# Optimization experiments

Measured on AMD Instinct MI355X. Metric: run time of the kernel, lower is better.

The kernel has to match this reference:

```python
import jax, jax.numpy as jnp
import numpy as np

H = 512   # hidden_dim
D = 512   # token feature dim (GRU input_size)
A = 256   # attn_dim
V = 10000 # vocab_size
TE = 256  # encoder timesteps
TD = 128  # decoder timesteps


def setup_inputs() -> dict:
    key = jax.random.key(0)
    ks = jax.random.split(key, 18)
    f = lambda k, shape, s: jax.random.normal(k, shape, jnp.float32) * s
    return {
        "x": f(ks[0], (1, TE, D), 1.0),
        "y": f(ks[1], (1, TD, D), 1.0),
        # encoder GRU params (PyTorch layout: gates [r|z|n] stacked)
        "Wi_e": f(ks[2], (3 * H, D), 0.04), "Wh_e": f(ks[3], (3 * H, H), 0.04),
        "bi_e": f(ks[4], (3 * H,), 0.04), "bh_e": f(ks[5], (3 * H,), 0.04),
        # decoder GRU params
        "Wi_d": f(ks[6], (3 * H, D), 0.04), "Wh_d": f(ks[7], (3 * H, H), 0.04),
        "bi_d": f(ks[8], (3 * H,), 0.04), "bh_d": f(ks[9], (3 * H,), 0.04),
        # additive attention params
        "Wh_attn": f(ks[10], (A, H), 0.06), "Ws_attn": f(ks[11], (A, H), 0.06),
        "b_attn": f(ks[12], (A,), 0.06), "v_attn": f(ks[13], (A,), 0.06),
        # output projections
        "W1": f(ks[14], (2 * V, 2 * H), 0.03), "b1": f(ks[15], (2 * V,), 0.03),
        "W2": f(ks[16], (V, 2 * V), 0.02), "b2": f(ks[17], (V,), 0.02),
    }


def _gru_gates(gi, gh, h):
    # gi/gh: [..., 3H] stacked input/hidden gate pre-activations, h: [..., H]
    ir, iz, inn = jnp.split(gi, 3, axis=-1)
    hr, hz, hn = jnp.split(gh, 3, axis=-1)
    r = jax.nn.sigmoid(ir + hr)
    z = jax.nn.sigmoid(iz + hz)
    n = jnp.tanh(inn + r * hn)
    return (1.0 - z) * n + z * h


def reference(x, y, Wi_e, Wh_e, bi_e, bh_e, Wi_d, Wh_d, bi_d, bh_d,
              Wh_attn, Ws_attn, b_attn, v_attn, W1, b1, W2, b2):
    X = x[0]  # [TE, D]
    Y = y[0]  # [TD, D]

    # Encoder: original calls self.encoder per single token with NO carried
    # hidden state, so each h_i is one GRU step from zero hidden. Vectorized:
    gi = X @ Wi_e.T + bi_e                      # [TE, 3H]
    gh = jnp.broadcast_to(bh_e, gi.shape)       # zero hidden -> only bias
    enc_H = _gru_gates(gi, gh, jnp.zeros((X.shape[0], H), X.dtype))  # [TE, H]
    h0 = enc_H[-1]                              # encoder_hidden_last

    # Decoder GRU over y with initial hidden h0
    def step(h, x_t):
        gi_t = x_t @ Wi_d.T + bi_d
        gh_t = h @ Wh_d.T + bh_d
        h_new = _gru_gates(gi_t, gh_t, h)
        return h_new, h_new

    _, dec_S = jax.lax.scan(step, h0, Y)        # [TD, H]

    # Bahdanau additive attention, fully batched over (TD, TE)
    encP = enc_H @ Wh_attn.T                    # [TE, A]
    decP = dec_S @ Ws_attn.T                    # [TD, A]
    e = jnp.tanh(encP[None, :, :] + decP[:, None, :] + b_attn)  # [TD, TE, A]
    scores = jnp.einsum('tea,a->te', e, v_attn)  # [TD, TE]
    attn = jax.nn.softmax(scores, axis=1)        # softmax over encoder steps
    context = attn @ enc_H                       # [TD, H]

    concat = jnp.concatenate([context, dec_S], axis=-1)  # [TD, 2H]
    out = concat @ W1.T + b1                     # [TD, 2V]
    out = out @ W2.T + b2                        # [TD, V]
    return out
```

## Files before the change

kernel.cpp:

```cpp
#include <hip/hip_runtime.h>
#include <stdint.h>

#define HID 512
#define THREE_H 1536
#define ADIM 256
#define NVOC 10000
#define TEnc 256
#define TDec 128

typedef float f32x4 __attribute__((ext_vector_type(4)));
typedef __bf16 bf16x8 __attribute__((ext_vector_type(8)));

__device__ __forceinline__ unsigned short f2bf(float f) {
  union { float f; unsigned u; } v; v.f = f;
  unsigned r = v.u + 0x7FFFu + ((v.u >> 16) & 1u);
  return (unsigned short)(r >> 16);
}
__device__ __forceinline__ float sigmoidf_(float x) { return 1.f / (1.f + __expf(-x)); }
__device__ __forceinline__ float tanh_fast(float x) {
  float ax = fabsf(x);
  float e = __expf(ax + ax);
  float t = 1.f - 2.f / (e + 1.f);
  return copysignf(t, x);
}

__device__ __forceinline__ void st_u64_sys(unsigned long long* p, unsigned long long v) {
  asm volatile("global_store_dwordx2 %0, %1, off sc0 sc1" :: "v"(p), "v"(v) : "memory");
}
__device__ __forceinline__ unsigned long long ld_u64_sys(const unsigned long long* p) {
  unsigned long long a;
  asm volatile("global_load_dwordx2 %0, %1, off sc0 sc1\n\ts_waitcnt vmcnt(0)"
               : "=&v"(a) : "v"(p) : "memory");
  return a;
}

#define GLDS16(gp, lp)                                                                 \
  __builtin_amdgcn_global_load_lds((const __attribute__((address_space(1))) void*)(gp),\
                                   (__attribute__((address_space(3))) void*)(lp), 16, 0, 0)

__global__ void cvt_xy(const float* __restrict__ x, const float* __restrict__ y,
                       unsigned short* __restrict__ xb, unsigned short* __restrict__ yb) {
  int i = (blockIdx.x * blockDim.x + threadIdx.x) * 4;
  const float* src;
  unsigned short* dst;
  int j;
  if (i < TEnc * HID) { src = x; dst = xb; j = i; }
  else { src = y; dst = yb; j = i - TEnc * HID; }
  float4 v = *(const float4*)(src + j);
  ushort4 o;
  o.x = f2bf(v.x); o.y = f2bf(v.y); o.z = f2bf(v.z); o.w = f2bf(v.w);
  *(ushort4*)(dst + j) = o;
}

template <int BN, int BK>
__global__ __launch_bounds__(256, 1) void gemm_bt(
    const unsigned short* __restrict__ Abf, const float* __restrict__ B,
    const float* __restrict__ bias, float* __restrict__ C, unsigned short* __restrict__ Cbf,
    int M, int N, int K) {
  constexpr int NF = BN / 16;
  constexpr int B4 = BN * BK / 1024;
  constexpr int AG = BK / 16;
  constexpr int KK = BK / 32;
  extern __shared__ char smem[];
  unsigned short* Al0 = (unsigned short*)smem;
  unsigned short* Al1 = Al0 + 128 * BK;
  unsigned short* Bl0 = Al1 + 128 * BK;
  unsigned short* Bl1 = Bl0 + BN * BK;

  const int tid = threadIdx.x;
  const int lane = tid & 63;
  const int wid = tid >> 6;
  const int m0 = blockIdx.x * 128;
  const int n0 = blockIdx.y * BN;
  const int NT = K / BK;

  float4 breg[B4];
  f32x4 acc[2][NF];
#pragma unroll
  for (int i = 0; i < 2; ++i)
#pragma unroll
    for (int j = 0; j < NF; ++j) acc[i][j] = (f32x4){0.f, 0.f, 0.f, 0.f};

  auto stageA = [&](int t, unsigned short* dst) {
    const unsigned short* Ab = Abf + (size_t)m0 * K + (size_t)t * BK;
#pragma unroll
    for (int g = 0; g < AG; ++g) {
      int elem = g * 2048 + tid * 8;
      int arow = elem / BK;
      int acol = elem - arow * BK;
      GLDS16(Ab + (size_t)arow * K + acol, (char*)dst + g * 4096 + wid * 1024);
    }
  };
  auto loadB = [&](int t) {
    const float* Bb = B + (size_t)t * BK;
#pragma unroll
    for (int p = 0; p < B4; ++p) {
      int e = (p * 256 + tid) * 4;
      int brow = e / BK;
      int bcol = e - brow * BK;
      int grow = n0 + brow;
      if (grow > N - 1) grow = N - 1;
      breg[p] = *(const float4*)(Bb + (size_t)grow * K + bcol);
    }
  };
  auto writeB = [&](unsigned short* dst) {
#pragma unroll
    for (int p = 0; p < B4; ++p) {
      ushort4 o;
      o.x = f2bf(breg[p].x); o.y = f2bf(breg[p].y);
      o.z = f2bf(breg[p].z); o.w = f2bf(breg[p].w);
      *(ushort4*)((char*)dst + (p * 256 + tid) * 8) = o;
    }
  };

  stageA(0, Al0);
  loadB(0);
  for (int t = 0; t < NT; ++t) {
    unsigned short* Ac = (t & 1) ? Al1 : Al0;
    unsigned short* Bc = (t & 1) ? Bl1 : Bl0;
    asm volatile("s_waitcnt vmcnt(0)" ::: "memory");
    writeB(Bc);
    __syncthreads();
    if (t + 1 < NT) {
      stageA(t + 1, (t & 1) ? Al0 : Al1);
      loadB(t + 1);
    }
    const int r0 = lane & 15;
    const int kb = (lane >> 4) * 8;
#pragma unroll
    for (int kk = 0; kk < KK; ++kk) {
      int ko = kk * 32 + kb;
      bf16x8 a0 = *(const bf16x8*)(Ac + (wid * 32 + r0) * BK + ko);
      bf16x8 a1 = *(const bf16x8*)(Ac + (wid * 32 + 16 + r0) * BK + ko);
#pragma unroll
      for (int nf = 0; nf < NF; ++nf) {
        bf16x8 bb = *(const bf16x8*)(Bc + (nf * 16 + r0) * BK + ko);
        acc[0][nf] = __builtin_amdgcn_mfma_f32_16x16x32_bf16(a0, bb, acc[0][nf], 0, 0, 0);
        acc[1][nf] = __builtin_amdgcn_mfma_f32_16x16x32_bf16(a1, bb, acc[1][nf], 0, 0, 0);
      }
    }
  }
  const int cc = lane & 15;
  const int rq = (lane >> 4) * 4;
#pragma unroll
  for (int mi = 0; mi < 2; ++mi) {
    int row = m0 + wid * 32 + mi * 16 + rq;
#pragma unroll
    for (int nf = 0; nf < NF; ++nf) {
      int col = n0 + nf * 16 + cc;
      if (col < N) {
        float bv = bias ? bias[col] : 0.f;
#pragma unroll
        for (int j = 0; j < 4; ++j) {
          float v = acc[mi][nf][j] + bv;
          if (C) C[(size_t)(row + j) * N + col] = v;
          if (Cbf) Cbf[(size_t)(row + j) * N + col] = f2bf(v);
        }
      }
    }
  }
}

__global__ __launch_bounds__(256, 1) void gemm_enc(
    const unsigned short* __restrict__ Abf, const float* __restrict__ Wi,
    const float* __restrict__ bi, const float* __restrict__ bh,
    float* __restrict__ encH, unsigned short* __restrict__ encHbf) {
  constexpr int BN = 96, BK = 128, NF = 6, B4 = 12, AG = 8, KK = 4, K = 512;
  extern __shared__ char smem[];
  unsigned short* Al0 = (unsigned short*)smem;
  unsigned short* Al1 = Al0 + 128 * BK;
  unsigned short* Bl0 = Al1 + 128 * BK;
  unsigned short* Bl1 = Bl0 + BN * BK;

  const int tid = threadIdx.x;
  const int lane = tid & 63;
  const int wid = tid >> 6;
  const int m0 = blockIdx.x * 128;
  const int n0g = blockIdx.y * 32;
  const int NT = K / BK;

  float4 breg[B4];
  f32x4 acc[2][NF];
#pragma unroll
  for (int i = 0; i < 2; ++i)
#pragma unroll
    for (int j = 0; j < NF; ++j) acc[i][j] = (f32x4){0.f, 0.f, 0.f, 0.f};

  auto stageA = [&](int t, unsigned short* dst) {
    const unsigned short* Ab = Abf + (size_t)m0 * K + (size_t)t * BK;
#pragma unroll
    for (int g = 0; g < AG; ++g) {
      int elem = g * 2048 + tid * 8;
      int arow = elem >> 7;
      int acol = elem & 127;
      GLDS16(Ab + (size_t)arow * K + acol, (char*)dst + g * 4096 + wid * 1024);
    }
  };
  auto loadB = [&](int t) {
    const float* Bb = Wi + (size_t)t * BK;
#pragma unroll
    for (int p = 0; p < B4; ++p) {
      int e = (p * 256 + tid) * 4;
      int brow = e >> 7;
      int bcol = e & 127;
      int grow = (brow >> 5) * HID + n0g + (brow & 31);
      breg[p] = *(const float4*)(Bb + (size_t)grow * K + bcol);
    }
  };
  auto writeB = [&](unsigned short* dst) {
#pragma unroll
    for (int p = 0; p < B4; ++p) {
      ushort4 o;
      o.x = f2bf(breg[p].x); o.y = f2bf(breg[p].y);
      o.z = f2bf(breg[p].z); o.w = f2bf(breg[p].w);
      *(ushort4*)((char*)dst + (p * 256 + tid) * 8) = o;
    }
  };

  stageA(0, Al0);
  loadB(0);
  for (int t = 0; t < NT; ++t) {
    unsigned short* Ac = (t & 1) ? Al1 : Al0;
    unsigned short* Bc = (t & 1) ? Bl1 : Bl0;
    asm volatile("s_waitcnt vmcnt(0)" ::: "memory");
    writeB(Bc);
    __syncthreads();
    if (t + 1 < NT) {
      stageA(t + 1, (t & 1) ? Al0 : Al1);
      loadB(t + 1);
    }
    const int r0 = lane & 15;
    const int kb = (lane >> 4) * 8;
#pragma unroll
    for (int kk = 0; kk < KK; ++kk) {
      int ko = kk * 32 + kb;
      bf16x8 a0 = *(const bf16x8*)(Ac + (wid * 32 + r0) * BK + ko);
      bf16x8 a1 = *(const bf16x8*)(Ac + (wid * 32 + 16 + r0) * BK + ko);
#pragma unroll
      for (int nf = 0; nf < NF; ++nf) {
        bf16x8 bb = *(const bf16x8*)(Bc + (nf * 16 + r0) * BK + ko);
        acc[0][nf] = __builtin_amdgcn_mfma_f32_16x16x32_bf16(a0, bb, acc[0][nf], 0, 0, 0);
        acc[1][nf] = __builtin_amdgcn_mfma_f32_16x16x32_bf16(a1, bb, acc[1][nf], 0, 0, 0);
      }
    }
  }
  const int cc = lane & 15;
  const int rq = (lane >> 4) * 4;
#pragma unroll
  for (int mi = 0; mi < 2; ++mi) {
    int row = m0 + wid * 32 + mi * 16 + rq;
#pragma unroll
    for (int nfj = 0; nfj < 2; ++nfj) {
      int j = n0g + nfj * 16 + cc;
      float br_ = bi[j] + bh[j];
      float bz_ = bi[HID + j] + bh[HID + j];
      float bin_ = bi[2 * HID + j];
      float bhn_ = bh[2 * HID + j];
#pragma unroll
      for (int jj = 0; jj < 4; ++jj) {
        float r = sigmoidf_(acc[mi][nfj][jj] + br_);
        float z = sigmoidf_(acc[mi][nfj + 2][jj] + bz_);
        float n = tanh_fast(acc[mi][nfj + 4][jj] + bin_ + r * bhn_);
        float h = (1.f - z) * n;
        encH[(size_t)(row + jj) * HID + j] = h;
        encHbf[(size_t)(row + jj) * HID + j] = f2bf(h);
      }
    }
  }
}

__global__ __launch_bounds__(256, 1) void gru_scan(
    const float* __restrict__ Whd, const float* __restrict__ bhd,
    const float* __restrict__ giY, const float* __restrict__ h0,
    unsigned long long* __restrict__ hx,
    unsigned short* __restrict__ decSbf, unsigned short* __restrict__ concatbf) {
  __shared__ float hl[548];
  __shared__ float dots[48];
  const int tid = threadIdx.x;
  const int lane = tid & 63, wid = tid >> 6;
  const int g = blockIdx.x;

  const int row16 = lane & 15;
  const int q = lane >> 4;
  float4 wreg[32];
  {
    int wrow = (wid < 3) ? wid : 0;
    const float* wr = Whd + ((size_t)wrow * HID + (size_t)g * 16 + row16) * HID + q * 128;
#pragma unroll
    for (int i = 0; i < 32; ++i) wreg[i] = *(const float4*)(wr + i * 4);
  }
  float bhr = 0.f, bhz = 0.f, bhn = 0.f, hreg = 0.f;
  if (wid == 3 && lane < 16) {
    int jj = g * 16 + lane;
    bhr = bhd[jj]; bhz = bhd[HID + jj]; bhn = bhd[2 * HID + jj];
    hreg = h0[jj];
  }
  {
    int w0 = tid * 2, w1 = tid * 2 + 1;
    hl[w0 + ((w0 >> 7) << 2)] = h0[w0];
    hl[w1 + ((w1 >> 7) << 2)] = h0[w1];
  }
  __syncthreads();

  for (int t = 0; t < TDec; ++t) {
    float gir = 0.f, giz = 0.f, gin = 0.f;
    if (wid < 3) {
      const float4* hp = (const float4*)hl;
      const int hb = q * 33;
      float p0 = 0.f, p1 = 0.f, p2 = 0.f, p3 = 0.f;
#pragma unroll
      for (int i = 0; i < 32; i += 4) {
        float4 ha = hp[hb + i], hv = hp[hb + i + 1], hc = hp[hb + i + 2], hd = hp[hb + i + 3];
        float4 wa = wreg[i], wb = wreg[i + 1], wc = wreg[i + 2], wd = wreg[i + 3];
        p0 += wa.x * ha.x + wa.y * ha.y + wa.z * ha.z + wa.w * ha.w;
        p1 += wb.x * hv.x + wb.y * hv.y + wb.z * hv.z + wb.w * hv.w;
        p2 += wc.x * hc.x + wc.y * hc.y + wc.z * hc.z + wc.w * hc.w;
        p3 += wd.x * hd.x + wd.y * hd.y + wd.z * hd.z + wd.w * hd.w;
      }
      float p = (p0 + p1) + (p2 + p3);
      p += __shfl_xor(p, 16);
      p += __shfl_xor(p, 32);
      if (lane < 16) dots[wid * 16 + lane] = p;
    } else if (lane < 16) {
      int jj = g * 16 + lane;
      const float* gi = giY + (size_t)t * THREE_H;
      gir = gi[jj]; giz = gi[HID + jj]; gin = gi[2 * HID + jj];
    }
    __syncthreads();
    unsigned long long* hxB = hx + (size_t)(t & 1) * 256;
    if (wid == 3 && lane < 16) {
      int jj = g * 16 + lane;
      float r = sigmoidf_(gir + dots[lane] + bhr);
      float z = sigmoidf_(giz + dots[16 + lane] + bhz);
      float n = tanh_fast(gin + r * (dots[32 + lane] + bhn));
      float hn = (1.f - z) * n + z * hreg;
      hreg = hn;
      unsigned short hb16 = f2bf(hn);
      unsigned short hb_up = (unsigned short)__shfl_xor((int)hb16, 1);
      if ((lane & 1) == 0) {
        unsigned long long w = ((unsigned long long)(unsigned)(t + 1) << 32) |
                               ((unsigned)hb_up << 16) | (unsigned)hb16;
        st_u64_sys(hxB + g * 8 + (lane >> 1), w);
      }
      decSbf[(size_t)t * HID + jj] = hb16;
      concatbf[(size_t)t * 2 * HID + HID + jj] = hb16;
    }
    if (t == TDec - 1) break;
    {
      const unsigned long long* p0 = hxB + tid;
      const unsigned tag = (unsigned)(t + 1);
      unsigned long long v;
      int guard = 0;
      do { v = ld_u64_sys(p0); } while ((unsigned)(v >> 32) != tag && ++guard < (1 << 20));
      int w0 = tid * 2, w1 = tid * 2 + 1;
      hl[w0 + ((w0 >> 7) << 2)] = __uint_as_float(((unsigned)v & 0xFFFFu) << 16);
      hl[w1 + ((w1 >> 7) << 2)] = __uint_as_float((((unsigned)v >> 16) & 0xFFFFu) << 16);
    }
    __syncthreads();
  }
}

__global__ __launch_bounds__(256) void attn_ctx(const float* __restrict__ encP,
                                                const float* __restrict__ decP,
                                                const float* __restrict__ vattn,
                                                const float* __restrict__ encH,
                                                unsigned short* __restrict__ concatbf) {
  __shared__ float dp[ADIM], vv[ADIM], pl[TEnc];
  __shared__ float red[8];
  const int t = blockIdx.x, tid = threadIdx.x;
  if (tid < 64) {
    *(float4*)(dp + tid * 4) = *(const float4*)(decP + (size_t)t * ADIM + tid * 4);
    *(float4*)(vv + tid * 4) = *(const float4*)(vattn + tid * 4);
  }
  __syncthreads();
  float s = 0.f;
  const float* ep = encP + (size_t)tid * ADIM;
#pragma unroll 4
  for (int a = 0; a < ADIM; a += 4) {
    float4 e4 = *(const float4*)(ep + a);
    s += vv[a] * tanh_fast(e4.x + dp[a]);
    s += vv[a + 1] * tanh_fast(e4.y + dp[a + 1]);
    s += vv[a + 2] * tanh_fast(e4.z + dp[a + 2]);
    s += vv[a + 3] * tanh_fast(e4.w + dp[a + 3]);
  }
  float m = s;
#pragma unroll
  for (int off = 32; off; off >>= 1) m = fmaxf(m, __shfl_xor(m, off));
  if ((tid & 63) == 0) red[tid >> 6] = m;
  __syncthreads();
  m = fmaxf(fmaxf(red[0], red[1]), fmaxf(red[2], red[3]));
  float p = __expf(s - m);
  pl[tid] = p;
  float sum = p;
#pragma unroll
  for (int off = 32; off; off >>= 1) sum += __shfl_xor(sum, off);
  if ((tid & 63) == 0) red[4 + (tid >> 6)] = sum;
  __syncthreads();
  float inv = 1.f / (red[4] + red[5] + red[6] + red[7]);
  float a0 = 0.f, a1 = 0.f;
  for (int e = 0; e < TEnc; ++e) {
    float pe = pl[e];
    a0 += pe * encH[(size_t)e * HID + tid];
    a1 += pe * encH[(size_t)e * HID + tid + 256];
  }
  concatbf[(size_t)t * 2 * HID + tid] = f2bf(a0 * inv);
  concatbf[(size_t)t * 2 * HID + tid + 256] = f2bf(a1 * inv);
}

extern "C" void kernel_launch(void* const* d_in, const int* in_sizes, int n_in,
                              void* d_out, int out_size, void* d_ws, size_t ws_size,
                              hipStream_t stream) {
  const float* x = (const float*)d_in[0];
  const float* y = (const float*)d_in[1];
  const float* Wi_e = (const float*)d_in[2];
  const float* bi_e = (const float*)d_in[4];
  const float* bh_e = (const float*)d_in[5];
  const float* Wi_d = (const float*)d_in[6];
  const float* Wh_d = (const float*)d_in[7];
  const float* bi_d = (const float*)d_in[8];
  const float* bh_d = (const float*)d_in[9];
  const float* Wh_attn = (const float*)d_in[10];
  const float* Ws_attn = (const float*)d_in[11];
  const float* b_attn = (const float*)d_in[12];
  const float* v_attn = (const float*)d_in[13];
  const float* W1 = (const float*)d_in[14];
  const float* b1 = (const float*)d_in[15];
  const float* W2 = (const float*)d_in[16];
  const float* b2 = (const float*)d_in[17];
  float* out = (float*)d_out;

  char* ws = (char*)d_ws;
  size_t off = 0;
  auto alloc = [&](size_t bytes) {
    char* p = ws + off;
    off += (bytes + 255) & ~(size_t)255;
    return p;
  };
  char* ctrl = alloc(4096);
  unsigned long long* hx = (unsigned long long*)ctrl;
  unsigned short* Xbf = (unsigned short*)alloc((size_t)TEnc * HID * 2);
  unsigned short* Ybf = (unsigned short*)alloc((size_t)TDec * HID * 2);
  float* giY = (float*)alloc((size_t)TDec * THREE_H * 4);
  float* encH = (float*)alloc((size_t)TEnc * HID * 4);
  unsigned short* encHbf = (unsigned short*)alloc((size_t)TEnc * HID * 2);
  float* encP = (float*)alloc((size_t)TEnc * ADIM * 4);
  float* decP = (float*)alloc((size_t)TDec * ADIM * 4);
  unsigned short* decSbf = (unsigned short*)alloc((size_t)TDec * HID * 2);
  unsigned short* concatbf = (unsigned short*)alloc((size_t)TDec * 2 * HID * 2);
  unsigned short* out1bf = (unsigned short*)alloc((size_t)TDec * 20000 * 2);

  hipMemsetAsync(ctrl, 0, 4096, stream);

  auto* g32 = gemm_bt<32, 128>;
  auto* g80 = gemm_bt<80, 128>;
  auto* g64 = gemm_bt<64, 160>;
  const int smem32 = (128 + 32) * 128 * 2 * 2;
  const int smem80 = (128 + 80) * 128 * 2 * 2;
  const int smem64 = (128 + 64) * 160 * 2 * 2;
  const int smemEnc = (128 + 96) * 128 * 2 * 2;
  hipFuncSetAttribute((const void*)g32, hipFuncAttributeMaxDynamicSharedMemorySize, smem32);
  hipFuncSetAttribute((const void*)g80, hipFuncAttributeMaxDynamicSharedMemorySize, smem80);
  hipFuncSetAttribute((const void*)g64, hipFuncAttributeMaxDynamicSharedMemorySize, smem64);
  hipFuncSetAttribute((const void*)gemm_enc, hipFuncAttributeMaxDynamicSharedMemorySize, smemEnc);

  cvt_xy<<<(TEnc + TDec) * HID / 1024, 256, 0, stream>>>(x, y, Xbf, Ybf);
  gemm_enc<<<dim3(2, 16), 256, smemEnc, stream>>>(Xbf, Wi_e, bi_e, bh_e, encH, encHbf);
  g32<<<dim3(2, 8), 256, smem32, stream>>>(encHbf, Wh_attn, nullptr, encP, nullptr, 256, 256, 512);
  g32<<<dim3(1, 48), 256, smem32, stream>>>(Ybf, Wi_d, bi_d, giY, nullptr, 128, 1536, 512);
  gru_scan<<<32, 256, 0, stream>>>(Wh_d, bh_d, giY, encH + 255 * HID, hx, decSbf, concatbf);
  g32<<<dim3(1, 8), 256, smem32, stream>>>(decSbf, Ws_attn, b_attn, decP, nullptr, 128, 256, 512);
  attn_ctx<<<TDec, 256, 0, stream>>>(encP, decP, v_attn, encH, concatbf);
  g80<<<dim3(1, 250), 256, smem80, stream>>>(concatbf, W1, b1, nullptr, out1bf, 128, 20000, 1024);
  g64<<<dim3(1, 157), 256, smem64, stream>>>(out1bf, W2, b2, out, nullptr, 128, NVOC, 20000);
}
```

Before: 601.1 us.

## Replicate GRU hidden-state mailbox per block and shrink W2 GEMM tile

The decoder GRU scan now writes each new hidden-state slice into 32 per-block copies of the exchange buffer. Each block polls its own private copy instead of all 32 blocks polling one shared buffer, which is meant to cut contention on the system-scope loads in the serial loop. The cost is 32 times more remote stores per step and a larger control buffer to clear. Separately, the final W2 GEMM tile width drops from 64 to 32 columns, doubling the grid to 313 blocks for better CU occupancy at the cost of less reuse of the A operand.

```diff
diff --git a/kernel.cpp b/kernel.cpp
--- a/kernel.cpp
+++ b/kernel.cpp
@@ -327,27 +327,35 @@
       gir = gi[jj]; giz = gi[HID + jj]; gin = gi[2 * HID + jj];
     }
     __syncthreads();
-    unsigned long long* hxB = hx + (size_t)(t & 1) * 256;
-    if (wid == 3 && lane < 16) {
-      int jj = g * 16 + lane;
-      float r = sigmoidf_(gir + dots[lane] + bhr);
-      float z = sigmoidf_(giz + dots[16 + lane] + bhz);
-      float n = tanh_fast(gin + r * (dots[32 + lane] + bhn));
-      float hn = (1.f - z) * n + z * hreg;
-      hreg = hn;
-      unsigned short hb16 = f2bf(hn);
-      unsigned short hb_up = (unsigned short)__shfl_xor((int)hb16, 1);
-      if ((lane & 1) == 0) {
-        unsigned long long w = ((unsigned long long)(unsigned)(t + 1) << 32) |
-                               ((unsigned)hb_up << 16) | (unsigned)hb16;
-        st_u64_sys(hxB + g * 8 + (lane >> 1), w);
-      }
-      decSbf[(size_t)t * HID + jj] = hb16;
-      concatbf[(size_t)t * 2 * HID + HID + jj] = hb16;
+    unsigned long long* hxB = hx + (size_t)(t & 1) * (32 * 256);
+    if (wid == 3) {
+      unsigned long long wval = 0;
+      if (lane < 16) {
+        int jj = g * 16 + lane;
+        float r = sigmoidf_(gir + dots[lane] + bhr);
+        float z = sigmoidf_(giz + dots[16 + lane] + bhz);
+        float n = tanh_fast(gin + r * (dots[32 + lane] + bhn));
+        float hn = (1.f - z) * n + z * hreg;
+        hreg = hn;
+        unsigned short hb16 = f2bf(hn);
+        unsigned short hb_up = (unsigned short)__shfl_xor((int)hb16, 1);
+        wval = ((unsigned long long)(unsigned)(t + 1) << 32) |
+               ((unsigned)hb_up << 16) | (unsigned)hb16;
+        decSbf[(size_t)t * HID + jj] = hb16;
+        concatbf[(size_t)t * 2 * HID + HID + jj] = hb16;
+      }
+      if (t < TDec - 1) {
+        unsigned long long bw = __shfl(wval, 2 * (lane & 7));
+        const int c0 = lane >> 3;
+        const int wofs = g * 8 + (lane & 7);
+#pragma unroll
+        for (int rep = 0; rep < 4; ++rep)
+          st_u64_sys(hxB + (size_t)(c0 + rep * 8) * 256 + wofs, bw);
+      }
     }
     if (t == TDec - 1) break;
     {
-      const unsigned long long* p0 = hxB + tid;
+      const unsigned long long* p0 = hxB + (size_t)g * 256 + tid;
       const unsigned tag = (unsigned)(t + 1);
       unsigned long long v;
       int guard = 0;
@@ -436,7 +444,7 @@
     off += (bytes + 255) & ~(size_t)255;
     return p;
   };
-  char* ctrl = alloc(4096);
+  char* ctrl = alloc(2 * 32 * 256 * 8);
   unsigned long long* hx = (unsigned long long*)ctrl;
   unsigned short* Xbf = (unsigned short*)alloc((size_t)TEnc * HID * 2);
   unsigned short* Ybf = (unsigned short*)alloc((size_t)TDec * HID * 2);
@@ -449,18 +457,18 @@
   unsigned short* concatbf = (unsigned short*)alloc((size_t)TDec * 2 * HID * 2);
   unsigned short* out1bf = (unsigned short*)alloc((size_t)TDec * 20000 * 2);
 
-  hipMemsetAsync(ctrl, 0, 4096, stream);
+  hipMemsetAsync(ctrl, 0, 2 * 32 * 256 * 8, stream);
 
   auto* g32 = gemm_bt<32, 128>;
   auto* g80 = gemm_bt<80, 128>;
-  auto* g64 = gemm_bt<64, 160>;
+  auto* gW2 = gemm_bt<32, 160>;
   const int smem32 = (128 + 32) * 128 * 2 * 2;
   const int smem80 = (128 + 80) * 128 * 2 * 2;
-  const int smem64 = (128 + 64) * 160 * 2 * 2;
+  const int smemW2 = (128 + 32) * 160 * 2 * 2;
   const int smemEnc = (128 + 96) * 128 * 2 * 2;
   hipFuncSetAttribute((const void*)g32, hipFuncAttributeMaxDynamicSharedMemorySize, smem32);
   hipFuncSetAttribute((const void*)g80, hipFuncAttributeMaxDynamicSharedMemorySize, smem80);
-  hipFuncSetAttribute((const void*)g64, hipFuncAttributeMaxDynamicSharedMemorySize, smem64);
+  hipFuncSetAttribute((const void*)gW2, hipFuncAttributeMaxDynamicSharedMemorySize, smemW2);
   hipFuncSetAttribute((const void*)gemm_enc, hipFuncAttributeMaxDynamicSharedMemorySize, smemEnc);
 
   cvt_xy<<<(TEnc + TDec) * HID / 1024, 256, 0, stream>>>(x, y, Xbf, Ybf);
@@ -471,5 +479,5 @@
   g32<<<dim3(1, 8), 256, smem32, stream>>>(decSbf, Ws_attn, b_attn, decP, nullptr, 128, 256, 512);
   attn_ctx<<<TDec, 256, 0, stream>>>(encP, decP, v_attn, encH, concatbf);
   g80<<<dim3(1, 250), 256, smem80, stream>>>(concatbf, W1, b1, nullptr, out1bf, 128, 20000, 1024);
-  g64<<<dim3(1, 157), 256, smem64, stream>>>(out1bf, W2, b2, out, nullptr, 128, NVOC, 20000);
-}
+  gW2<<<dim3(1, 313), 256, smemW2, stream>>>(out1bf, W2, b2, out, nullptr, 128, NVOC, 20000);
+}
```

Result: slower. 812.2 us (+35.1%).

## Prefetch output weights during GRU scan and fuse decoder attention projection

Applied to the files above, without the earlier changes.

Extra blocks are appended to the sequential GRU scan launch that stream W1 and part of W2 from memory, so these weights may be cache-resident when the output GEMMs run, using otherwise idle CUs during the latency-bound recurrence. The separate decP GEMM launch is removed; attn_ctx now computes the decoder-state projection with Ws_attn itself from the bf16 decoder states. The prefetch traffic could interfere with the scan's cross-block polling, and the fused projection recomputes per block in fp32 scalar code.

```diff
diff --git a/kernel.cpp b/kernel.cpp
--- a/kernel.cpp
+++ b/kernel.cpp
@@ -273,12 +273,41 @@
     const float* __restrict__ Whd, const float* __restrict__ bhd,
     const float* __restrict__ giY, const float* __restrict__ h0,
     unsigned long long* __restrict__ hx,
-    unsigned short* __restrict__ decSbf, unsigned short* __restrict__ concatbf) {
+    unsigned short* __restrict__ decSbf, unsigned short* __restrict__ concatbf,
+    const float* __restrict__ W1w, const float* __restrict__ W2w) {
   __shared__ float hl[548];
   __shared__ float dots[48];
   const int tid = threadIdx.x;
   const int lane = tid & 63, wid = tid >> 6;
   const int g = blockIdx.x;
+
+  if (g >= 32) {
+    const int widx = g - 32;
+    float keep = 0.f;
+    {
+      const float4* s2 = (const float4*)(W2w + (size_t)widx * 7 * 20000);
+      const int n4 = 7 * 20000 / 4;
+      for (int i = tid; i < n4; i += 256) {
+        float4 v = s2[i];
+        keep += v.x + v.y + v.z + v.w;
+        if ((i & 1023) == tid) __builtin_amdgcn_s_sleep(127);
+      }
+    }
+    {
+      const float4* s1 = (const float4*)(W1w + (size_t)widx * 96 * 1024);
+      const int n4 = 96 * 1024 / 4;
+      const size_t base4 = (size_t)widx * 96 * 1024 / 4;
+      const size_t lim4 = (size_t)20000 * 1024 / 4;
+      for (int i = tid; i < n4; i += 256) {
+        if (base4 + i >= lim4) break;
+        float4 v = s1[i];
+        keep += v.x + v.y + v.z + v.w;
+        if ((i & 1023) == tid) __builtin_amdgcn_s_sleep(127);
+      }
+    }
+    asm volatile("" :: "v"(keep));
+    return;
+  }
 
   const int row16 = lane & 15;
   const int q = lane >> 4;
@@ -361,16 +390,37 @@
 }
 
 __global__ __launch_bounds__(256) void attn_ctx(const float* __restrict__ encP,
-                                                const float* __restrict__ decP,
+                                                const unsigned short* __restrict__ decSbf,
+                                                const float* __restrict__ Ws,
+                                                const float* __restrict__ battn,
                                                 const float* __restrict__ vattn,
                                                 const float* __restrict__ encH,
                                                 unsigned short* __restrict__ concatbf) {
-  __shared__ float dp[ADIM], vv[ADIM], pl[TEnc];
+  __shared__ float dp[ADIM], vv[ADIM], pl[TEnc], dsr[HID];
   __shared__ float red[8];
   const int t = blockIdx.x, tid = threadIdx.x;
-  if (tid < 64) {
-    *(float4*)(dp + tid * 4) = *(const float4*)(decP + (size_t)t * ADIM + tid * 4);
-    *(float4*)(vv + tid * 4) = *(const float4*)(vattn + tid * 4);
+  {
+    unsigned short u0 = decSbf[(size_t)t * HID + tid];
+    unsigned short u1 = decSbf[(size_t)t * HID + tid + 256];
+    dsr[tid] = __uint_as_float((unsigned)u0 << 16);
+    dsr[tid + 256] = __uint_as_float((unsigned)u1 << 16);
+  }
+  if (tid < 64) *(float4*)(vv + tid * 4) = *(const float4*)(vattn + tid * 4);
+  __syncthreads();
+  {
+    const float4* wr = (const float4*)(Ws + (size_t)tid * HID);
+    const float4* hr = (const float4*)dsr;
+    float s0 = 0.f, s1 = 0.f, s2 = 0.f, s3 = 0.f;
+#pragma unroll 4
+    for (int k = 0; k < 128; k += 4) {
+      float4 w0 = wr[k], w1 = wr[k + 1], w2 = wr[k + 2], w3 = wr[k + 3];
+      float4 h0 = hr[k], h1 = hr[k + 1], h2 = hr[k + 2], h3 = hr[k + 3];
+      s0 += w0.x * h0.x + w0.y * h0.y + w0.z * h0.z + w0.w * h0.w;
+      s1 += w1.x * h1.x + w1.y * h1.y + w1.z * h1.z + w1.w * h1.w;
+      s2 += w2.x * h2.x + w2.y * h2.y + w2.z * h2.z + w2.w * h2.w;
+      s3 += w3.x * h3.x + w3.y * h3.y + w3.z * h3.z + w3.w * h3.w;
+    }
+    dp[tid] = (s0 + s1) + (s2 + s3) + battn[tid];
   }
   __syncthreads();
   float s = 0.f;
@@ -444,7 +494,6 @@
   float* encH = (float*)alloc((size_t)TEnc * HID * 4);
   unsigned short* encHbf = (unsigned short*)alloc((size_t)TEnc * HID * 2);
   float* encP = (float*)alloc((size_t)TEnc * ADIM * 4);
-  float* decP = (float*)alloc((size_t)TDec * ADIM * 4);
   unsigned short* decSbf = (unsigned short*)alloc((size_t)TDec * HID * 2);
   unsigned short* concatbf = (unsigned short*)alloc((size_t)TDec * 2 * HID * 2);
   unsigned short* out1bf = (unsigned short*)alloc((size_t)TDec * 20000 * 2);
@@ -467,9 +516,9 @@
   gemm_enc<<<dim3(2, 16), 256, smemEnc, stream>>>(Xbf, Wi_e, bi_e, bh_e, encH, encHbf);
   g32<<<dim3(2, 8), 256, smem32, stream>>>(encHbf, Wh_attn, nullptr, encP, nullptr, 256, 256, 512);
   g32<<<dim3(1, 48), 256, smem32, stream>>>(Ybf, Wi_d, bi_d, giY, nullptr, 128, 1536, 512);
-  gru_scan<<<32, 256, 0, stream>>>(Wh_d, bh_d, giY, encH + 255 * HID, hx, decSbf, concatbf);
-  g32<<<dim3(1, 8), 256, smem32, stream>>>(decSbf, Ws_attn, b_attn, decP, nullptr, 128, 256, 512);
-  attn_ctx<<<TDec, 256, 0, stream>>>(encP, decP, v_attn, encH, concatbf);
+  gru_scan<<<241, 256, 0, stream>>>(Wh_d, bh_d, giY, encH + 255 * HID, hx,
+                                    decSbf, concatbf, W1, W2);
+  attn_ctx<<<TDec, 256, 0, stream>>>(encP, decSbf, Ws_attn, b_attn, v_attn, encH, concatbf);
   g80<<<dim3(1, 250), 256, smem80, stream>>>(concatbf, W1, b1, nullptr, out1bf, 128, 20000, 1024);
   g64<<<dim3(1, 157), 256, smem64, stream>>>(out1bf, W2, b2, out, nullptr, 128, NVOC, 20000);
 }
```

Result: slower. 660.7 us (+9.9%).
